# Kernel optimization log

Hardware: AMD Instinct MI355X
Metric: run time of the kernel (lower is better)

The kernel has to match this reference:

```python
import jax, jax.numpy as jnp
import numpy as np

EPS = 1e-6
ALPHA = 0.1
BETA = 0.25


def setup_inputs() -> dict:
    key = jax.random.key(0)
    k1, k2, k3 = jax.random.split(key, 3)
    B, C, D = 4096, 256, 128
    x = jax.random.normal(k1, (B, D), dtype=jnp.float32)
    prev_q = jax.random.normal(k2, (B, D), dtype=jnp.float32)
    codes = jax.random.normal(k3, (1, C, D), dtype=jnp.float32)
    return {"x": x, "prev_q": prev_q, "codes": codes}


def compute_distance(x, codes):
    # x: (B, D); codes: (1, C, D) or (B, 1, D) -> (B, C) / (B, 1); metric='l2'
    return jnp.sum((x[:, None, :] - codes) ** 2, axis=-1)


def get_rotation_matrix(u, v, eps=EPS):
    # u: (B, D) normalized; v: (D,) normalized -> R: (B, D, D)
    B, D = u.shape
    uvT = u[:, :, None] * v[None, None, :]          # (B, D, D) = u v^T
    vuT = v[None, :, None] * u[:, None, :]          # (B, D, D) = v u^T
    A = uvT - vuT
    A2 = jnp.einsum('bik,bkj->bij', A, A)
    dot = jnp.einsum('bd,d->b', u, v)[:, None, None]
    I = jnp.eye(D, dtype=u.dtype)
    return I + A + A2 / (1.0 + dot + eps)


def reference(x, prev_q, codes):
    B, D = x.shape
    v = jnp.ones((D,), dtype=x.dtype) / jnp.sqrt(jnp.asarray(D, x.dtype))
    # F.normalize(prev_q, dim=-1, eps=1e-6)
    n = jnp.linalg.norm(prev_q, axis=-1, keepdims=True)
    u = prev_q / jnp.maximum(n, EPS)
    R = get_rotation_matrix(u, v)
    # x_canonical = R^T x
    x_canonical = jnp.einsum('bji,bj->bi', R, x)
    raw_distances = compute_distance(x_canonical, codes)        # (B, C)
    distances = raw_distances / D / ALPHA
    # eval path: argmin + gather
    indices = jnp.argmin(distances, axis=-1)                    # (B,)
    quantized_canonical = codes[0][indices]                     # (B, D)
    quantized = jnp.einsum('bij,bj->bi', R, quantized_canonical)
    loss_commit = compute_distance(x, jax.lax.stop_gradient(quantized)[:, None, :]).mean()
    loss_codebook = compute_distance(jax.lax.stop_gradient(x), quantized[:, None, :]).mean()
    loss = loss_commit + BETA * loss_codebook
    return quantized, indices, loss
```

## Files before the change

kernel.cpp:

```cpp
#include <hip/hip_runtime.h>

#define BD 4096
#define CD 256
#define DD 128
#define RB 16
#define SF 132

__global__ __launch_bounds__(256) void rq_fused(
    const float* __restrict__ x,
    const float* __restrict__ pq,
    const float* __restrict__ codes,
    float* __restrict__ out)
{
    __shared__ float code_s[CD * SF];
    __shared__ float xc_s[RB * SF];
    __shared__ float row_c[RB], row_s[RB], row_invn[RB];
    __shared__ int   row_idx[RB];
    __shared__ float red_v[RB * 2];
    __shared__ int   red_i[RB * 2];
    __shared__ float loss_s[RB];

    const int tid  = threadIdx.x;
    const int wv   = tid >> 6;
    const int lane = tid & 63;
    const int row0 = blockIdx.x * RB;
    const float INV_SQRT_D = 0.088388347648318447f;

    {
        const float4* src = (const float4*)codes;
        for (int k = 0; k < 32; k += 4) {
            const float4 t0 = src[(k + 0) * 256 + tid];
            const float4 t1 = src[(k + 1) * 256 + tid];
            const float4 t2 = src[(k + 2) * 256 + tid];
            const float4 t3 = src[(k + 3) * 256 + tid];
            int f;
            f = (k + 0) * 256 + tid; *(float4*)(code_s + (f >> 5) * SF + (f & 31) * 4) = t0;
            f = (k + 1) * 256 + tid; *(float4*)(code_s + (f >> 5) * SF + (f & 31) * 4) = t1;
            f = (k + 2) * 256 + tid; *(float4*)(code_s + (f >> 5) * SF + (f & 31) * 4) = t2;
            f = (k + 3) * 256 + tid; *(float4*)(code_s + (f >> 5) * SF + (f & 31) * 4) = t3;
        }
    }

    #pragma unroll
    for (int rr = 0; rr < 4; ++rr) {
        const int r = wv * 4 + rr;
        const size_t grow = (size_t)(row0 + r);
        const float2 xv = ((const float2*)(x  + grow * DD))[lane];
        const float2 pv = ((const float2*)(pq + grow * DD))[lane];
        float s0 = pv.x * pv.x + pv.y * pv.y;
        float s1 = pv.x + pv.y;
        float s2 = xv.x + xv.y;
        float s3 = pv.x * xv.x + pv.y * xv.y;
        #pragma unroll
        for (int m = 32; m > 0; m >>= 1) {
            s0 += __shfl_xor(s0, m);
            s1 += __shfl_xor(s1, m);
            s2 += __shfl_xor(s2, m);
            s3 += __shfl_xor(s3, m);
        }
        const float invn = 1.0f / fmaxf(sqrtf(s0), 1e-6f);
        const float b = s2 * INV_SQRT_D;
        const float a = s3 * invn;
        const float c = s1 * invn * INV_SQRT_D;
        const float s = 1.0f / (1.0f + c + 1e-6f);
        const float au = -b + s * (c * b - a);
        const float av =  a + s * (c * a - b);
        xc_s[r * SF + 2 * lane]     = xv.x + au * (pv.x * invn) + av * INV_SQRT_D;
        xc_s[r * SF + 2 * lane + 1] = xv.y + au * (pv.y * invn) + av * INV_SQRT_D;
        if (lane == 0) { row_c[r] = c; row_s[r] = s; row_invn[r] = invn; }
    }
    __syncthreads();

    const int rbase = (wv >> 1) * 8;
    const int cbase = (wv & 1) * 128;
    const float* cp0 = code_s + (cbase + lane) * SF;
    const float* cp1 = cp0 + 64 * SF;
    const float* xb  = xc_s + rbase * SF;
    float acc[16];
    #pragma unroll
    for (int j = 0; j < 16; ++j) acc[j] = 0.f;

    #pragma unroll 2
    for (int i = 0; i < 32; ++i) {
        const float4 q0 = *(const float4*)(cp0 + i * 4);
        const float4 q1 = *(const float4*)(cp1 + i * 4);
        #pragma unroll
        for (int rr = 0; rr < 8; ++rr) {
            const float4 xv = *(const float4*)(xb + rr * SF + i * 4);
            float dx;
            dx = xv.x - q0.x; acc[rr * 2]     = fmaf(dx, dx, acc[rr * 2]);
            dx = xv.y - q0.y; acc[rr * 2]     = fmaf(dx, dx, acc[rr * 2]);
            dx = xv.z - q0.z; acc[rr * 2]     = fmaf(dx, dx, acc[rr * 2]);
            dx = xv.w - q0.w; acc[rr * 2]     = fmaf(dx, dx, acc[rr * 2]);
            dx = xv.x - q1.x; acc[rr * 2 + 1] = fmaf(dx, dx, acc[rr * 2 + 1]);
            dx = xv.y - q1.y; acc[rr * 2 + 1] = fmaf(dx, dx, acc[rr * 2 + 1]);
            dx = xv.z - q1.z; acc[rr * 2 + 1] = fmaf(dx, dx, acc[rr * 2 + 1]);
            dx = xv.w - q1.w; acc[rr * 2 + 1] = fmaf(dx, dx, acc[rr * 2 + 1]);
        }
    }

    float bv[8]; int bi[8];
    #pragma unroll
    for (int rr = 0; rr < 8; ++rr) {
        const float v0 = acc[rr * 2], v1 = acc[rr * 2 + 1];
        if (v1 < v0) { bv[rr] = v1; bi[rr] = cbase + 64 + lane; }
        else         { bv[rr] = v0; bi[rr] = cbase + lane; }
    }
    #pragma unroll
    for (int m = 1; m < 64; m <<= 1) {
        #pragma unroll
        for (int rr = 0; rr < 8; ++rr) {
            const float ov = __shfl_xor(bv[rr], m);
            const int   oi = __shfl_xor(bi[rr], m);
            if (ov < bv[rr] || (ov == bv[rr] && oi < bi[rr])) { bv[rr] = ov; bi[rr] = oi; }
        }
    }
    if (lane == 0) {
        #pragma unroll
        for (int rr = 0; rr < 8; ++rr) {
            red_v[(rbase + rr) * 2 + (wv & 1)] = bv[rr];
            red_i[(rbase + rr) * 2 + (wv & 1)] = bi[rr];
        }
    }
    __syncthreads();
    if (tid < RB) {
        float v0 = red_v[tid * 2]; int i0 = red_i[tid * 2];
        const float v1 = red_v[tid * 2 + 1]; const int i1 = red_i[tid * 2 + 1];
        if (v1 < v0 || (v1 == v0 && i1 < i0)) { v0 = v1; i0 = i1; }
        row_idx[tid] = i0;
        out[(size_t)BD * DD + row0 + tid] = (float)i0;
    }
    __syncthreads();

    #pragma unroll
    for (int rr = 0; rr < 4; ++rr) {
        const int r = wv * 4 + rr;
        const int qi = row_idx[r];
        const float invn = row_invn[r];
        const float c = row_c[r];
        const float s = row_s[r];
        const size_t grow = (size_t)(row0 + r);
        const float2 q = ((const float2*)(code_s + qi * SF))[lane];
        const float2 p = ((const float2*)(pq + grow * DD))[lane];
        float pd = p.x * q.x + p.y * q.y;
        float ws = q.x + q.y;
        #pragma unroll
        for (int m = 32; m > 0; m >>= 1) {
            pd += __shfl_xor(pd, m);
            ws += __shfl_xor(ws, m);
        }
        const float pp = pd * invn;
        const float w  = ws * INV_SQRT_D;
        const float bu  =  w + s * (c * w - pp);
        const float bvv = -pp + s * (c * pp - w);
        float2 o;
        o.x = q.x + bu * (p.x * invn) + bvv * INV_SQRT_D;
        o.y = q.y + bu * (p.y * invn) + bvv * INV_SQRT_D;
        ((float2*)(out + grow * DD))[lane] = o;

        const float2 xv = ((const float2*)(x + grow * DD))[lane];
        float dx = xv.x - o.x;
        float ls = dx * dx;
        dx = xv.y - o.y;
        ls = fmaf(dx, dx, ls);
        #pragma unroll
        for (int m = 32; m > 0; m >>= 1) ls += __shfl_xor(ls, m);
        if (lane == 0) loss_s[r] = ls;
    }
    __syncthreads();
    if (tid == 0) {
        float tot = 0.f;
        #pragma unroll
        for (int r = 0; r < RB; ++r) tot += loss_s[r];
        atomicAdd(out + (size_t)BD * DD + BD, tot * (1.25f / (float)BD));
    }
}

extern "C" void kernel_launch(void* const* d_in, const int* in_sizes, int n_in,
                              void* d_out, int out_size, void* d_ws, size_t ws_size,
                              hipStream_t stream) {
    const float* xin   = (const float*)d_in[0];
    const float* prevq = (const float*)d_in[1];
    const float* codes = (const float*)d_in[2];
    float* out = (float*)d_out;
    hipMemsetAsync((void*)(out + (size_t)BD * DD + BD), 0, sizeof(float), stream);
    rq_fused<<<BD / RB, 256, 0, stream>>>(xin, prevq, codes, out);
}
```

Baseline: 80.99 us.

## Use 1024-thread blocks with one row per wave and finer distance split

Raises the block size from 256 to 1024 threads so each of the 16 waves handles one row in the prologue and epilogue. In the distance phase each wave now covers 4 rows against 64 codes instead of 8 rows against 128, cutting per-thread accumulators and work. Reduction shared arrays grow to merge four code-quarter partials. This trades register reuse of code vectors (more LDS reads per FMA) for more waves per block to hide latency, and the 135KB LDS footprint still limits residency to one block per CU.

```diff
diff --git a/kernel.cpp b/kernel.cpp
--- a/kernel.cpp
+++ b/kernel.cpp
@@ -4,9 +4,10 @@
 #define CD 256
 #define DD 128
 #define RB 16
+#define TB 1024
 #define SF 132
 
-__global__ __launch_bounds__(256) void rq_fused(
+__global__ __launch_bounds__(TB) void rq_fused(
     const float* __restrict__ x,
     const float* __restrict__ pq,
     const float* __restrict__ codes,
@@ -16,8 +17,8 @@
     __shared__ float xc_s[RB * SF];
     __shared__ float row_c[RB], row_s[RB], row_invn[RB];
     __shared__ int   row_idx[RB];
-    __shared__ float red_v[RB * 2];
-    __shared__ int   red_i[RB * 2];
+    __shared__ float red_v[RB * 4];
+    __shared__ int   red_i[RB * 4];
     __shared__ float loss_s[RB];
 
     const int tid  = threadIdx.x;
@@ -28,22 +29,22 @@
 
     {
         const float4* src = (const float4*)codes;
-        for (int k = 0; k < 32; k += 4) {
-            const float4 t0 = src[(k + 0) * 256 + tid];
-            const float4 t1 = src[(k + 1) * 256 + tid];
-            const float4 t2 = src[(k + 2) * 256 + tid];
-            const float4 t3 = src[(k + 3) * 256 + tid];
+        #pragma unroll
+        for (int k = 0; k < 8; k += 4) {
+            const float4 t0 = src[(k + 0) * TB + tid];
+            const float4 t1 = src[(k + 1) * TB + tid];
+            const float4 t2 = src[(k + 2) * TB + tid];
+            const float4 t3 = src[(k + 3) * TB + tid];
             int f;
-            f = (k + 0) * 256 + tid; *(float4*)(code_s + (f >> 5) * SF + (f & 31) * 4) = t0;
-            f = (k + 1) * 256 + tid; *(float4*)(code_s + (f >> 5) * SF + (f & 31) * 4) = t1;
-            f = (k + 2) * 256 + tid; *(float4*)(code_s + (f >> 5) * SF + (f & 31) * 4) = t2;
-            f = (k + 3) * 256 + tid; *(float4*)(code_s + (f >> 5) * SF + (f & 31) * 4) = t3;
+            f = (k + 0) * TB + tid; *(float4*)(code_s + (f >> 5) * SF + (f & 31) * 4) = t0;
+            f = (k + 1) * TB + tid; *(float4*)(code_s + (f >> 5) * SF + (f & 31) * 4) = t1;
+            f = (k + 2) * TB + tid; *(float4*)(code_s + (f >> 5) * SF + (f & 31) * 4) = t2;
+            f = (k + 3) * TB + tid; *(float4*)(code_s + (f >> 5) * SF + (f & 31) * 4) = t3;
         }
     }
 
-    #pragma unroll
-    for (int rr = 0; rr < 4; ++rr) {
-        const int r = wv * 4 + rr;
+    {
+        const int r = wv;
         const size_t grow = (size_t)(row0 + r);
         const float2 xv = ((const float2*)(x  + grow * DD))[lane];
         const float2 pv = ((const float2*)(pq + grow * DD))[lane];
@@ -71,45 +72,45 @@
     }
     __syncthreads();
 
-    const int rbase = (wv >> 1) * 8;
-    const int cbase = (wv & 1) * 128;
-    const float* cp0 = code_s + (cbase + lane) * SF;
-    const float* cp1 = cp0 + 64 * SF;
-    const float* xb  = xc_s + rbase * SF;
-    float acc[16];
-    #pragma unroll
-    for (int j = 0; j < 16; ++j) acc[j] = 0.f;
+    const int rg = wv & 3;
+    const int cq = wv >> 2;
+    const int ci = cq * 64 + lane;
+    const float* cp = code_s + ci * SF;
+    const float* xb = xc_s + (rg * 4) * SF;
+    float a0 = 0.f, a1 = 0.f, a2 = 0.f, a3 = 0.f;
 
-    #pragma unroll 2
+    #pragma unroll 4
     for (int i = 0; i < 32; ++i) {
-        const float4 q0 = *(const float4*)(cp0 + i * 4);
-        const float4 q1 = *(const float4*)(cp1 + i * 4);
-        #pragma unroll
-        for (int rr = 0; rr < 8; ++rr) {
-            const float4 xv = *(const float4*)(xb + rr * SF + i * 4);
-            float dx;
-            dx = xv.x - q0.x; acc[rr * 2]     = fmaf(dx, dx, acc[rr * 2]);
-            dx = xv.y - q0.y; acc[rr * 2]     = fmaf(dx, dx, acc[rr * 2]);
-            dx = xv.z - q0.z; acc[rr * 2]     = fmaf(dx, dx, acc[rr * 2]);
-            dx = xv.w - q0.w; acc[rr * 2]     = fmaf(dx, dx, acc[rr * 2]);
-            dx = xv.x - q1.x; acc[rr * 2 + 1] = fmaf(dx, dx, acc[rr * 2 + 1]);
-            dx = xv.y - q1.y; acc[rr * 2 + 1] = fmaf(dx, dx, acc[rr * 2 + 1]);
-            dx = xv.z - q1.z; acc[rr * 2 + 1] = fmaf(dx, dx, acc[rr * 2 + 1]);
-            dx = xv.w - q1.w; acc[rr * 2 + 1] = fmaf(dx, dx, acc[rr * 2 + 1]);
-        }
+        const float4 q  = *(const float4*)(cp + i * 4);
+        const float4 v0 = *(const float4*)(xb + 0 * SF + i * 4);
+        const float4 v1 = *(const float4*)(xb + 1 * SF + i * 4);
+        const float4 v2 = *(const float4*)(xb + 2 * SF + i * 4);
+        const float4 v3 = *(const float4*)(xb + 3 * SF + i * 4);
+        float dx;
+        dx = v0.x - q.x; a0 = fmaf(dx, dx, a0);
+        dx = v0.y - q.y; a0 = fmaf(dx, dx, a0);
+        dx = v0.z - q.z; a0 = fmaf(dx, dx, a0);
+        dx = v0.w - q.w; a0 = fmaf(dx, dx, a0);
+        dx = v1.x - q.x; a1 = fmaf(dx, dx, a1);
+        dx = v1.y - q.y; a1 = fmaf(dx, dx, a1);
+        dx = v1.z - q.z; a1 = fmaf(dx, dx, a1);
+        dx = v1.w - q.w; a1 = fmaf(dx, dx, a1);
+        dx = v2.x - q.x; a2 = fmaf(dx, dx, a2);
+        dx = v2.y - q.y; a2 = fmaf(dx, dx, a2);
+        dx = v2.z - q.z; a2 = fmaf(dx, dx, a2);
+        dx = v2.w - q.w; a2 = fmaf(dx, dx, a2);
+        dx = v3.x - q.x; a3 = fmaf(dx, dx, a3);
+        dx = v3.y - q.y; a3 = fmaf(dx, dx, a3);
+        dx = v3.z - q.z; a3 = fmaf(dx, dx, a3);
+        dx = v3.w - q.w; a3 = fmaf(dx, dx, a3);
     }
 
-    float bv[8]; int bi[8];
-    #pragma unroll
-    for (int rr = 0; rr < 8; ++rr) {
-        const float v0 = acc[rr * 2], v1 = acc[rr * 2 + 1];
-        if (v1 < v0) { bv[rr] = v1; bi[rr] = cbase + 64 + lane; }
-        else         { bv[rr] = v0; bi[rr] = cbase + lane; }
-    }
+    float bv[4] = {a0, a1, a2, a3};
+    int   bi[4] = {ci, ci, ci, ci};
     #pragma unroll
     for (int m = 1; m < 64; m <<= 1) {
         #pragma unroll
-        for (int rr = 0; rr < 8; ++rr) {
+        for (int rr = 0; rr < 4; ++rr) {
             const float ov = __shfl_xor(bv[rr], m);
             const int   oi = __shfl_xor(bi[rr], m);
             if (ov < bv[rr] || (ov == bv[rr] && oi < bi[rr])) { bv[rr] = ov; bi[rr] = oi; }
@@ -117,24 +118,27 @@
     }
     if (lane == 0) {
         #pragma unroll
-        for (int rr = 0; rr < 8; ++rr) {
-            red_v[(rbase + rr) * 2 + (wv & 1)] = bv[rr];
-            red_i[(rbase + rr) * 2 + (wv & 1)] = bi[rr];
+        for (int rr = 0; rr < 4; ++rr) {
+            red_v[(rg * 4 + rr) * 4 + cq] = bv[rr];
+            red_i[(rg * 4 + rr) * 4 + cq] = bi[rr];
         }
     }
     __syncthreads();
     if (tid < RB) {
-        float v0 = red_v[tid * 2]; int i0 = red_i[tid * 2];
-        const float v1 = red_v[tid * 2 + 1]; const int i1 = red_i[tid * 2 + 1];
-        if (v1 < v0 || (v1 == v0 && i1 < i0)) { v0 = v1; i0 = i1; }
+        float v0 = red_v[tid * 4]; int i0 = red_i[tid * 4];
+        #pragma unroll
+        for (int k = 1; k < 4; ++k) {
+            const float ov = red_v[tid * 4 + k];
+            const int   oi = red_i[tid * 4 + k];
+            if (ov < v0 || (ov == v0 && oi < i0)) { v0 = ov; i0 = oi; }
+        }
         row_idx[tid] = i0;
         out[(size_t)BD * DD + row0 + tid] = (float)i0;
     }
     __syncthreads();
 
-    #pragma unroll
-    for (int rr = 0; rr < 4; ++rr) {
-        const int r = wv * 4 + rr;
+    {
+        const int r = wv;
         const int qi = row_idx[r];
         const float invn = row_invn[r];
         const float c = row_c[r];
@@ -184,5 +188,5 @@
     const float* codes = (const float*)d_in[2];
     float* out = (float*)d_out;
     hipMemsetAsync((void*)(out + (size_t)BD * DD + BD), 0, sizeof(float), stream);
-    rq_fused<<<BD / RB, 256, 0, stream>>>(xin, prevq, codes, out);
+    rq_fused<<<BD / RB, TB, 0, stream>>>(xin, prevq, codes, out);
 }
```

After: 77.47 us. 4.3% less time.
